# Performance work log

Measured on AMD Instinct MI355X. Metric: run time of the kernel, lower is better.

The kernel has to match this reference:

```python
import jax, jax.numpy as jnp
import numpy as np

N_NODES = 100000
N_EDGES = 1600000
D = 128
HID = 256  # min(2*D, 256)
D_OUT = 128
BN_EPS = 1e-5


def setup_inputs() -> dict:
    key = jax.random.key(0)
    ks = jax.random.split(key, 16)
    s = 0.05
    inp = {
        "x": jax.random.normal(ks[0], (N_NODES, D), dtype=jnp.float32),
        "edges": jax.random.randint(ks[1], (2, N_EDGES), 0, N_NODES, dtype=jnp.int32),
        # affine_before_rnn: Linear(D, D)
        "W_aff": jax.random.normal(ks[2], (D, D), dtype=jnp.float32) * s,
        "b_aff": jnp.zeros((D,), dtype=jnp.float32),
        # GRUCell(D, D)
        "W_ih": jax.random.normal(ks[3], (3 * D, D), dtype=jnp.float32) * s,
        "b_ih": jnp.zeros((3 * D,), dtype=jnp.float32),
        "W_hh": jax.random.normal(ks[4], (3 * D, D), dtype=jnp.float32) * s,
        "b_hh": jnp.zeros((3 * D,), dtype=jnp.float32),
        # merge_layer: Linear(2*D, D)
        "W_merge": jax.random.normal(ks[5], (D, 2 * D), dtype=jnp.float32) * s,
        "b_merge": jnp.zeros((D,), dtype=jnp.float32),
        # learnable self-connection weight
        "eps": jnp.asarray(1.0, dtype=jnp.float32),
        # backbone: Linear(D, HID) -> relu -> Linear(HID, D_OUT) -> relu -> BatchNorm1d
        "W1": jax.random.normal(ks[6], (HID, D), dtype=jnp.float32) * s,
        "b1": jnp.zeros((HID,), dtype=jnp.float32),
        "W2": jax.random.normal(ks[7], (D_OUT, HID), dtype=jnp.float32) * s,
        "b2": jnp.zeros((D_OUT,), dtype=jnp.float32),
        "gamma": jnp.ones((D_OUT,), dtype=jnp.float32),
        "beta": jnp.zeros((D_OUT,), dtype=jnp.float32),
    }
    return inp


def reference(x, edges, W_aff, b_aff, W_ih, b_ih, W_hh, b_hh,
              W_merge, b_merge, eps, W1, b1, W2, b2, gamma, beta):
    src, dst = edges[0], edges[1]
    n = x.shape[0]

    # ---- aggregation 1: 'sum' -> scatter-sum of neighbor features ----
    agg_sum = jax.ops.segment_sum(x[src], dst, num_segments=n)  # (N, D)

    # ---- aggregation 2: 'rnn-max' -> affine, scatter-max, GRUCell ----
    xi = x @ W_aff.T + b_aff
    agg_max = jax.ops.segment_max(xi[src], dst, num_segments=n)  # (N, D)
    agg_max = jnp.where(jnp.isfinite(agg_max), agg_max, 0.0)  # empty segments -> 0

    # GRUCell: input = aggregated neighbors, hidden = original node features
    gi = agg_max @ W_ih.T + b_ih  # (N, 3D)
    gh = x @ W_hh.T + b_hh        # (N, 3D)
    ir, iz, inn = jnp.split(gi, 3, axis=1)
    hr, hz, hn = jnp.split(gh, 3, axis=1)
    r = jax.nn.sigmoid(ir + hr)
    z = jax.nn.sigmoid(iz + hz)
    ncand = jnp.tanh(inn + r * hn)
    rnn_out = (1.0 - z) * ncand + z * x  # (N, D)

    # ---- merge ('cat') ----
    h = jnp.concatenate([agg_sum, rnn_out], axis=1) @ W_merge.T + b_merge  # (N, D)

    # ---- learnable self-connection ----
    h = h + eps * x

    # ---- backbone: dense -> relu -> dense -> relu -> batchnorm1d (train mode) ----
    h = jax.nn.relu(h @ W1.T + b1)
    h = jax.nn.relu(h @ W2.T + b2)
    mean = jnp.mean(h, axis=0)
    var = jnp.mean(jnp.square(h - mean), axis=0)  # biased batch variance
    out = gamma * (h - mean) * jax.lax.rsqrt(var + BN_EPS) + beta
    return out
```

## Files before the change

kernel.cpp:

```cpp
#include <hip/hip_runtime.h>
#include <hip/hip_bf16.h>
#include <math.h>

using bf16 = __hip_bfloat16;
typedef __attribute__((ext_vector_type(8))) short bf16x8;
typedef __attribute__((ext_vector_type(4))) float f32x4;

__device__ __forceinline__ float b2f(unsigned short u) {
  return __uint_as_float(((unsigned)u) << 16);
}
__device__ __forceinline__ unsigned short f2b(float f) {
  bf16 h = __float2bfloat16(f);
  return *reinterpret_cast<unsigned short*>(&h);
}
__device__ __forceinline__ ushort4 f2b4(float4 v) {
  return make_ushort4(f2b(v.x), f2b(v.y), f2b(v.z), f2b(v.w));
}

__global__ __launch_bounds__(256) void mgemm_k(
    const unsigned short* __restrict__ A, int lda, const float* __restrict__ W,
    const float* __restrict__ bias, unsigned short* __restrict__ Cb, int ldc,
    int N, int M, int K) {
  constexpr int LDA = 72;
  __shared__ unsigned short As[128 * LDA];
  __shared__ unsigned short Ws[128 * LDA];

  const int tid = threadIdx.x;
  const int lane = tid & 63;
  const int wave = tid >> 6;
  const int row0 = blockIdx.y * 128;
  const int m0 = blockIdx.x * 128;
  const int rowhalf = (wave & 1) * 64;
  const int colhalf = (wave >> 1) * 64;
  const int l15 = lane & 15;
  const int quad = lane >> 4;

  f32x4 acc[4][4] = {};

  for (int kc = 0; kc < K; kc += 64) {
#pragma unroll
    for (int i = 0; i < 4; i++) {
      int idx = tid + i * 256;
      int r = idx >> 3;
      int k8 = (idx & 7) * 8;
      int row = row0 + r;
      ushort4 u0 = make_ushort4(0, 0, 0, 0), u1 = u0;
      if (row < N) {
        const unsigned short* s = A + (size_t)row * lda + kc + k8;
        u0 = *(const ushort4*)s;
        u1 = *(const ushort4*)(s + 4);
      }
      *(ushort4*)&As[r * LDA + k8] = u0;
      *(ushort4*)&As[r * LDA + k8 + 4] = u1;
    }
#pragma unroll
    for (int i = 0; i < 8; i++) {
      int idx = tid + i * 256;
      int r = idx >> 4;
      int k4 = idx & 15;
      float4 v = *(const float4*)(W + (size_t)(m0 + r) * K + kc + k4 * 4);
      *(ushort4*)&Ws[r * LDA + k4 * 4] = f2b4(v);
    }
    __syncthreads();
#pragma unroll
    for (int ks = 0; ks < 2; ks++) {
      const int ko = ks * 32 + quad * 8;
      bf16x8 af[4], wf[4];
#pragma unroll
      for (int ri = 0; ri < 4; ri++)
        af[ri] = *(const bf16x8*)&As[(rowhalf + ri * 16 + l15) * LDA + ko];
#pragma unroll
      for (int ci = 0; ci < 4; ci++)
        wf[ci] = *(const bf16x8*)&Ws[(colhalf + ci * 16 + l15) * LDA + ko];
#pragma unroll
      for (int ri = 0; ri < 4; ri++)
#pragma unroll
        for (int ci = 0; ci < 4; ci++)
          acc[ri][ci] = __builtin_amdgcn_mfma_f32_16x16x32_bf16(
              af[ri], wf[ci], acc[ri][ci], 0, 0, 0);
    }
    __syncthreads();
  }
#pragma unroll
  for (int ci = 0; ci < 4; ci++) {
    const int col = m0 + colhalf + ci * 16 + l15;
    const float bv = bias[col];
#pragma unroll
    for (int ri = 0; ri < 4; ri++) {
      const int rbase = row0 + rowhalf + ri * 16 + quad * 4;
#pragma unroll
      for (int r = 0; r < 4; r++) {
        int row = rbase + r;
        if (row >= N) continue;
        Cb[(size_t)row * ldc + col] = f2b(acc[ri][ci][r] + bv);
      }
    }
  }
}

__global__ __launch_bounds__(256, 4) void grubb_k(
    const unsigned short* __restrict__ aggm,
    const unsigned short* __restrict__ xcat,
    const unsigned short* __restrict__ aggs,
    const unsigned short* __restrict__ Wbig,
    const float* __restrict__ bias_big,
    const unsigned short* __restrict__ Wmb, const float* __restrict__ bm,
    const unsigned short* __restrict__ W1b, const float* __restrict__ b1,
    const unsigned short* __restrict__ W2b, const float* __restrict__ b2,
    const float* __restrict__ epsp, float* __restrict__ out,
    float* __restrict__ pstats, int N) {
  constexpr int LDA = 264;
  constexpr int LDH = 136;
  __shared__ unsigned short As[32 * LDA];
  __shared__ unsigned short Acat[32 * LDA];
  __shared__ float sbn[128], qbn[128];
  unsigned short* Hd = As;
  unsigned short* Hp = Acat;

  const int tid = threadIdx.x;
  const int lane = tid & 63;
  const int wave = tid >> 6;
  const int l15 = lane & 15;
  const int quad = lane >> 4;
  const int row0 = blockIdx.x * 32;
  if (tid < 128) {
    sbn[tid] = 0.f;
    qbn[tid] = 0.f;
  }
  const float ep = epsp[0];

  {
    int r = tid >> 3;
    int k32 = (tid & 7) * 32;
    int row = row0 + r;
    uint4 u[4] = {};
    uint4 v[2] = {};
    if (row < N) {
      const unsigned short* s = (k32 < 128)
                                    ? aggm + (size_t)row * 128 + k32
                                    : xcat + (size_t)row * 256 + (k32 - 128);
#pragma unroll
      for (int i = 0; i < 4; i++) u[i] = *(const uint4*)(s + i * 8);
      const unsigned short* s2 = aggs + (size_t)row * 128 + (tid & 7) * 16;
      v[0] = *(const uint4*)s2;
      v[1] = *(const uint4*)(s2 + 8);
    }
#pragma unroll
    for (int i = 0; i < 4; i++) *(uint4*)&As[r * LDA + k32 + i * 8] = u[i];
    int k16 = (tid & 7) * 16;
    *(uint4*)&Acat[r * LDA + k16] = v[0];
    *(uint4*)&Acat[r * LDA + k16 + 8] = v[1];
  }
  __syncthreads();

  {
    const unsigned short* wptr =
        Wbig + (size_t)(wave * 128 + l15) * 256 + quad * 8;
    f32x4 acc[2][8] = {};
    bf16x8 wfA[4], wfB[4];
#pragma unroll
    for (int ci = 0; ci < 4; ci++)
      wfA[ci] = *(const bf16x8*)(wptr + ci * 16 * 256);
#pragma unroll
    for (int ks = 0; ks < 8; ks++) {
      const int ko = ks * 32 + quad * 8;
      bf16x8 af0 = *(const bf16x8*)&As[l15 * LDA + ko];
      bf16x8 af1 = *(const bf16x8*)&As[(16 + l15) * LDA + ko];
#pragma unroll
      for (int ci = 0; ci < 4; ci++)
        wfB[ci] = *(const bf16x8*)(wptr + (ci + 4) * 16 * 256 + ks * 32);
#pragma unroll
      for (int ci = 0; ci < 4; ci++) {
        acc[0][ci] = __builtin_amdgcn_mfma_f32_16x16x32_bf16(af0, wfA[ci],
                                                             acc[0][ci], 0, 0, 0);
        acc[1][ci] = __builtin_amdgcn_mfma_f32_16x16x32_bf16(af1, wfA[ci],
                                                             acc[1][ci], 0, 0, 0);
      }
      if (ks < 7) {
#pragma unroll
        for (int ci = 0; ci < 4; ci++)
          wfA[ci] = *(const bf16x8*)(wptr + ci * 16 * 256 + (ks + 1) * 32);
      }
#pragma unroll
      for (int ci = 0; ci < 4; ci++) {
        acc[0][4 + ci] = __builtin_amdgcn_mfma_f32_16x16x32_bf16(
            af0, wfB[ci], acc[0][4 + ci], 0, 0, 0);
        acc[1][4 + ci] = __builtin_amdgcn_mfma_f32_16x16x32_bf16(
            af1, wfB[ci], acc[1][4 + ci], 0, 0, 0);
      }
    }
#pragma unroll
    for (int fi = 0; fi < 2; fi++) {
      const int f = wave * 32 + fi * 16 + l15;
      const float br = bias_big[f];
      const float bz = bias_big[128 + f];
      const float bi = bias_big[256 + f];
      const float bh = bias_big[384 + f];
#pragma unroll
      for (int ri = 0; ri < 2; ri++) {
#pragma unroll
        for (int r = 0; r < 4; r++) {
          int rl = ri * 16 + quad * 4 + r;
          float rg = 1.f / (1.f + __expf(-(acc[ri][4 * fi + 0][r] + br)));
          float zg = 1.f / (1.f + __expf(-(acc[ri][4 * fi + 1][r] + bz)));
          float a =
              acc[ri][4 * fi + 2][r] + bi + rg * (acc[ri][4 * fi + 3][r] + bh);
          float t = 1.f - 2.f / (__expf(2.f * fabsf(a)) + 1.f);
          float nc = copysignf(t, a);
          float xv = b2f(As[rl * LDA + 128 + f]);
          Acat[rl * LDA + 128 + f] = f2b((1.f - zg) * nc + zg * xv);
        }
      }
    }
  }
  __syncthreads();

  f32x4 accm[2][2] = {};
  {
    const unsigned short* wptr =
        Wmb + (size_t)(wave * 32 + l15) * 256 + quad * 8;
    bf16x8 w0 = *(const bf16x8*)(wptr);
    bf16x8 w1 = *(const bf16x8*)(wptr + 16 * 256);
#pragma unroll
    for (int ks = 0; ks < 8; ks++) {
      const int ko = ks * 32 + quad * 8;
      bf16x8 af[2];
#pragma unroll
      for (int ri = 0; ri < 2; ri++)
        af[ri] = *(const bf16x8*)&Acat[(ri * 16 + l15) * LDA + ko];
      bf16x8 n0, n1;
      if (ks < 7) {
        n0 = *(const bf16x8*)(wptr + (ks + 1) * 32);
        n1 = *(const bf16x8*)(wptr + 16 * 256 + (ks + 1) * 32);
      }
#pragma unroll
      for (int ri = 0; ri < 2; ri++) {
        accm[ri][0] = __builtin_amdgcn_mfma_f32_16x16x32_bf16(af[ri], w0,
                                                              accm[ri][0], 0, 0, 0);
        accm[ri][1] = __builtin_amdgcn_mfma_f32_16x16x32_bf16(af[ri], w1,
                                                              accm[ri][1], 0, 0, 0);
      }
      if (ks < 7) {
        w0 = n0;
        w1 = n1;
      }
    }
  }
  __syncthreads();
  {
#pragma unroll
    for (int ci = 0; ci < 2; ci++) {
      int c = wave * 32 + ci * 16 + l15;
      float bv = bm[c];
#pragma unroll
      for (int ri = 0; ri < 2; ri++) {
#pragma unroll
        for (int r = 0; r < 4; r++) {
          int rl = ri * 16 + quad * 4 + r;
          float v = accm[ri][ci][r] + bv + ep * b2f(As[rl * LDA + 128 + c]);
          Hp[rl * LDH + c] = f2b(v);
        }
      }
    }
  }
  __syncthreads();

  f32x4 acc3[2][2] = {};
#pragma unroll
  for (int hh = 0; hh < 2; hh++) {
    f32x4 acc2[2][2] = {};
    {
      const unsigned short* wptr =
          W1b + (size_t)(hh * 128 + wave * 32 + l15) * 128 + quad * 8;
      bf16x8 w0 = *(const bf16x8*)(wptr);
      bf16x8 w1 = *(const bf16x8*)(wptr + 16 * 128);
#pragma unroll
      for (int ks = 0; ks < 4; ks++) {
        const int ko = ks * 32 + quad * 8;
        bf16x8 af[2];
#pragma unroll
        for (int ri = 0; ri < 2; ri++)
          af[ri] = *(const bf16x8*)&Hp[(ri * 16 + l15) * LDH + ko];
        bf16x8 n0, n1;
        if (ks < 3) {
          n0 = *(const bf16x8*)(wptr + (ks + 1) * 32);
          n1 = *(const bf16x8*)(wptr + 16 * 128 + (ks + 1) * 32);
        }
#pragma unroll
        for (int ri = 0; ri < 2; ri++) {
          acc2[ri][0] = __builtin_amdgcn_mfma_f32_16x16x32_bf16(
              af[ri], w0, acc2[ri][0], 0, 0, 0);
          acc2[ri][1] = __builtin_amdgcn_mfma_f32_16x16x32_bf16(
              af[ri], w1, acc2[ri][1], 0, 0, 0);
        }
        if (ks < 3) {
          w0 = n0;
          w1 = n1;
        }
      }
    }
    __syncthreads();
#pragma unroll
    for (int ci = 0; ci < 2; ci++) {
      int c = wave * 32 + ci * 16 + l15;
      float bv = b1[hh * 128 + c];
#pragma unroll
      for (int ri = 0; ri < 2; ri++) {
#pragma unroll
        for (int r = 0; r < 4; r++) {
          int rl = ri * 16 + quad * 4 + r;
          Hd[rl * LDH + c] = f2b(fmaxf(acc2[ri][ci][r] + bv, 0.f));
        }
      }
    }
    __syncthreads();
    {
      const unsigned short* wptr =
          W2b + (size_t)(wave * 32 + l15) * 256 + hh * 128 + quad * 8;
      bf16x8 w0 = *(const bf16x8*)(wptr);
      bf16x8 w1 = *(const bf16x8*)(wptr + 16 * 256);
#pragma unroll
      for (int ks = 0; ks < 4; ks++) {
        const int ko = ks * 32 + quad * 8;
        bf16x8 af[2];
#pragma unroll
        for (int ri = 0; ri < 2; ri++)
          af[ri] = *(const bf16x8*)&Hd[(ri * 16 + l15) * LDH + ko];
        bf16x8 n0, n1;
        if (ks < 3) {
          n0 = *(const bf16x8*)(wptr + (ks + 1) * 32);
          n1 = *(const bf16x8*)(wptr + 16 * 256 + (ks + 1) * 32);
        }
#pragma unroll
        for (int ri = 0; ri < 2; ri++) {
          acc3[ri][0] = __builtin_amdgcn_mfma_f32_16x16x32_bf16(
              af[ri], w0, acc3[ri][0], 0, 0, 0);
          acc3[ri][1] = __builtin_amdgcn_mfma_f32_16x16x32_bf16(
              af[ri], w1, acc3[ri][1], 0, 0, 0);
        }
        if (ks < 3) {
          w0 = n0;
          w1 = n1;
        }
      }
    }
  }
#pragma unroll
  for (int ci = 0; ci < 2; ci++) {
    int c = wave * 32 + ci * 16 + l15;
    float bv = b2[c];
    float s = 0.f, q = 0.f;
#pragma unroll
    for (int ri = 0; ri < 2; ri++) {
#pragma unroll
      for (int r = 0; r < 4; r++) {
        int rl = ri * 16 + quad * 4 + r;
        int row = row0 + rl;
        if (row >= N) continue;
        float v = fmaxf(acc3[ri][ci][r] + bv, 0.f);
        out[(size_t)row * 128 + c] = v;
        s += v;
        q += v * v;
      }
    }
    atomicAdd(&sbn[c], s);
    atomicAdd(&qbn[c], q);
  }
  __syncthreads();
  if (tid < 128) {
    float* p = pstats + (size_t)blockIdx.x * 256;
    p[tid] = sbn[tid];
    p[128 + tid] = qbn[tid];
  }
}

__global__ __launch_bounds__(256) void bnred_k(const float* __restrict__ pstats,
                                               float* __restrict__ stats,
                                               int nb) {
  int t = threadIdx.x;
  float s = 0.f;
  for (int b = blockIdx.x; b < nb; b += gridDim.x)
    s += pstats[(size_t)b * 256 + t];
  atomicAdd(&stats[t], s);
}

__global__ __launch_bounds__(256) void prep_k(
    const float* __restrict__ W_ih, const float* __restrict__ b_ih,
    const float* __restrict__ W_hh, const float* __restrict__ b_hh,
    const float* __restrict__ Wm, const float* __restrict__ W1,
    const float* __restrict__ W2, unsigned short* __restrict__ Wbig,
    unsigned short* __restrict__ Wmb, unsigned short* __restrict__ W1b,
    unsigned short* __restrict__ W2b, float* __restrict__ bias_big,
    float* __restrict__ stats, int* __restrict__ deg, int N) {
  int idx = blockIdx.x * 256 + threadIdx.x;
  if (idx < N) deg[idx] = 0;
  if (idx < 32768) {
    int mp = idx >> 6;
    int k4 = (idx & 63) * 4;
    int w = mp >> 7, ci = (mp >> 4) & 7, l15 = mp & 15;
    int g = ci & 3, fi = ci >> 2;
    int f = w * 32 + fi * 16 + l15;
    const float* src = nullptr;
    int koff = 0;
    if (g <= 1) {
      int m = g * 128 + f;
      if (k4 < 128) { src = W_ih + (size_t)m * 128; koff = k4; }
      else          { src = W_hh + (size_t)m * 128; koff = k4 - 128; }
    } else if (g == 2) {
      if (k4 < 128) { src = W_ih + (size_t)(256 + f) * 128; koff = k4; }
    } else {
      if (k4 >= 128) { src = W_hh + (size_t)(256 + f) * 128; koff = k4 - 128; }
    }
    ushort4 o = make_ushort4(0, 0, 0, 0);
    if (src) o = f2b4(*(const float4*)(src + koff));
    *(ushort4*)&Wbig[(size_t)mp * 256 + k4] = o;
  }
  if (idx < 8192) {
    int m = idx >> 6;
    int k4 = (idx & 63) * 4;
    *(ushort4*)&Wmb[(size_t)m * 256 + k4] =
        f2b4(*(const float4*)(Wm + (size_t)m * 256 + k4));
    *(ushort4*)&W2b[(size_t)m * 256 + k4] =
        f2b4(*(const float4*)(W2 + (size_t)m * 256 + k4));
    int m2 = idx >> 5;
    int k42 = (idx & 31) * 4;
    *(ushort4*)&W1b[(size_t)m2 * 128 + k42] =
        f2b4(*(const float4*)(W1 + (size_t)m2 * 128 + k42));
  }
  if (blockIdx.x == 0) {
    int t = threadIdx.x;
    stats[t] = 0.f;
#pragma unroll
    for (int h = 0; h < 2; h++) {
      int mm = t + h * 256;
      float b;
      if (mm < 256) b = b_ih[mm] + b_hh[mm];
      else if (mm < 384) b = b_ih[mm];
      else b = b_hh[mm - 128];
      bias_big[mm] = b;
    }
  }
}

__global__ __launch_bounds__(256) void cvthist_k(
    const int* __restrict__ edges, int* __restrict__ deg, int E,
    const float* __restrict__ x, unsigned short* __restrict__ xcat,
    int ngroups, int eblk) {
  if ((int)blockIdx.x < eblk) {
    int e = blockIdx.x * 256 + threadIdx.x;
    if (e < E) atomicAdd(&deg[edges[(size_t)E + e]], 1);
  } else {
    int g = (blockIdx.x - eblk) * 256 + threadIdx.x;
    if (g >= ngroups) return;
    int n = g >> 5;
    int j = (g & 31) * 4;
    float4 v = *(const float4*)&x[(size_t)n * 128 + j];
    *(ushort4*)&xcat[(size_t)n * 256 + j] = f2b4(v);
  }
}

__global__ __launch_bounds__(256) void scan1_k(const int* __restrict__ deg,
                                               int* __restrict__ off,
                                               int* __restrict__ bsums, int N) {
  __shared__ int s[256];
  int t = threadIdx.x;
  int i = blockIdx.x * 256 + t;
  int v = (i < N) ? deg[i] : 0;
  s[t] = v;
  __syncthreads();
#pragma unroll
  for (int d = 1; d < 256; d <<= 1) {
    int u = (t >= d) ? s[t - d] : 0;
    __syncthreads();
    s[t] += u;
    __syncthreads();
  }
  if (i < N) off[i] = s[t] - v;
  if (t == 255) bsums[blockIdx.x] = s[255];
}

__global__ __launch_bounds__(512) void scan2_k(int* __restrict__ bsums,
                                               int nb) {
  __shared__ int s[512];
  int t = threadIdx.x;
  int v = (t < nb) ? bsums[t] : 0;
  s[t] = v;
  __syncthreads();
#pragma unroll
  for (int d = 1; d < 512; d <<= 1) {
    int u = (t >= d) ? s[t - d] : 0;
    __syncthreads();
    s[t] += u;
    __syncthreads();
  }
  if (t < nb) bsums[t] = s[t] - v;
}

__global__ __launch_bounds__(256) void scan3_k(int* __restrict__ off,
                                               const int* __restrict__ bsums,
                                               int* __restrict__ binoff,
                                               int* __restrict__ bincur,
                                               int N, int E, int NB) {
  int i = blockIdx.x * 256 + threadIdx.x;
  if (i < N) {
    int o = off[i] + bsums[blockIdx.x];
    off[i] = o;
    if ((i & 511) == 0) {
      binoff[i >> 9] = o;
      bincur[i >> 9] = o;
    }
  }
  if (i == 0) {
    off[N] = E;
    binoff[NB] = E;
  }
}

__global__ __launch_bounds__(256) void edgepart_k(const int* __restrict__ edges,
                                                  int* __restrict__ bincur,
                                                  int* __restrict__ part,
                                                  int E, int NB) {
  __shared__ int cnt[256];
  const int tid = threadIdx.x;
  if (tid < NB) cnt[tid] = 0;
  __syncthreads();
  int sv[16], dv[16];
  const int e0 = blockIdx.x * 4096;
#pragma unroll
  for (int i = 0; i < 16; i++) {
    int e = e0 + i * 256 + tid;
    int s = 0, d = -1;
    if (e < E) {
      s = edges[e];
      d = edges[(size_t)E + e];
    }
    sv[i] = s;
    dv[i] = d;
    if (d >= 0) atomicAdd(&cnt[d >> 9], 1);
  }
  __syncthreads();
  if (tid < NB) {
    int c = cnt[tid];
    int base = c ? atomicAdd(&bincur[tid], c) : 0;
    cnt[tid] = base;
  }
  __syncthreads();
#pragma unroll
  for (int i = 0; i < 16; i++) {
    int d = dv[i];
    if (d < 0) continue;
    int p = atomicAdd(&cnt[d >> 9], 1);
    part[p] = (sv[i] << 9) | (d & 511);
  }
}

__global__ __launch_bounds__(1024) void fill2_k(const int* __restrict__ off,
                                                const int* __restrict__ binoff,
                                                const int* __restrict__ part,
                                                int* __restrict__ bucket,
                                                int N) {
  __shared__ int scur[512];
  const int b = blockIdx.x;
  const int n0 = b << 9;
  const int tid = threadIdx.x;
  if (tid < 512) {
    int node = n0 + tid;
    scur[tid] = (node < N) ? off[node] : 0;
  }
  __syncthreads();
  const int j0 = binoff[b];
  const int j1 = binoff[b + 1];
  for (int j = j0 + tid; j < j1; j += 1024) {
    int p = part[j];
    int pos = atomicAdd(&scur[p & 511], 1);
    bucket[pos] = p >> 9;
  }
}

__global__ __launch_bounds__(256) void gather_k(
    const int* __restrict__ off, const int* __restrict__ bucket,
    const unsigned short* __restrict__ xcat, unsigned short* __restrict__ aggm,
    unsigned short* __restrict__ aggs, int N) {
  int node = blockIdx.x * 4 + (threadIdx.x >> 6);
  if (node >= N) return;
  const int lane = threadIdx.x & 63;
  const int half = lane >> 5;
  const int f = (lane & 31) * 4;
  const int j0 = off[node], jend = off[node + 1];
  float s0 = 0.f, s1 = 0.f, s2 = 0.f, s3 = 0.f;
  float m0 = -INFINITY, m1 = -INFINITY, m2 = -INFINITY, m3 = -INFINITY;
  int jj = j0 + half;
  int p0 = (jj < jend) ? bucket[jj] : 0;
  int p1 = (jj + 2 < jend) ? bucket[jj + 2] : 0;
  for (; jj < jend; jj += 2) {
    int src = p0;
    p0 = p1;
    p1 = (jj + 4 < jend) ? bucket[jj + 4] : 0;
    ushort4 a = *(const ushort4*)(xcat + (size_t)src * 256 + f);
    ushort4 b = *(const ushort4*)(xcat + (size_t)src * 256 + 128 + f);
    s0 += b2f(a.x);
    s1 += b2f(a.y);
    s2 += b2f(a.z);
    s3 += b2f(a.w);
    m0 = fmaxf(m0, b2f(b.x));
    m1 = fmaxf(m1, b2f(b.y));
    m2 = fmaxf(m2, b2f(b.z));
    m3 = fmaxf(m3, b2f(b.w));
  }
  s0 += __shfl_xor(s0, 32);
  s1 += __shfl_xor(s1, 32);
  s2 += __shfl_xor(s2, 32);
  s3 += __shfl_xor(s3, 32);
  m0 = fmaxf(m0, __shfl_xor(m0, 32));
  m1 = fmaxf(m1, __shfl_xor(m1, 32));
  m2 = fmaxf(m2, __shfl_xor(m2, 32));
  m3 = fmaxf(m3, __shfl_xor(m3, 32));
  if (half == 0) {
    bool nz = jend > j0;
    ushort4 mv = nz ? make_ushort4(f2b(m0), f2b(m1), f2b(m2), f2b(m3))
                    : make_ushort4(0, 0, 0, 0);
    *(ushort4*)&aggm[(size_t)node * 128 + f] = mv;
    *(ushort4*)&aggs[(size_t)node * 128 + f] =
        make_ushort4(f2b(s0), f2b(s1), f2b(s2), f2b(s3));
  }
}

__global__ __launch_bounds__(256) void bn_apply_k(
    float* __restrict__ out, const float* __restrict__ stats,
    const float* __restrict__ gamma, const float* __restrict__ beta,
    float invn, int nd4) {
  int g = blockIdx.x * 256 + threadIdx.x;
  if (g >= nd4) return;
  int d = (g & 31) * 4;
  float4 v = ((float4*)out)[g];
  float o[4] = {v.x, v.y, v.z, v.w};
#pragma unroll
  for (int i = 0; i < 4; i++) {
    float mean = stats[d + i] * invn;
    float var = fmaxf(stats[128 + d + i] * invn - mean * mean, 0.f);
    float sc = gamma[d + i] * rsqrtf(var + 1e-5f);
    o[i] = (o[i] - mean) * sc + beta[d + i];
  }
  ((float4*)out)[g] = make_float4(o[0], o[1], o[2], o[3]);
}

extern "C" void kernel_launch(void* const* d_in, const int* in_sizes, int n_in,
                              void* d_out, int out_size, void* d_ws,
                              size_t ws_size, hipStream_t stream) {
  (void)n_in;
  (void)out_size;
  (void)ws_size;
  const float* x = (const float*)d_in[0];
  const int* edges = (const int*)d_in[1];
  const float* W_aff = (const float*)d_in[2];
  const float* b_aff = (const float*)d_in[3];
  const float* W_ih = (const float*)d_in[4];
  const float* b_ih = (const float*)d_in[5];
  const float* W_hh = (const float*)d_in[6];
  const float* b_hh = (const float*)d_in[7];
  const float* W_merge = (const float*)d_in[8];
  const float* b_merge = (const float*)d_in[9];
  const float* epsp = (const float*)d_in[10];
  const float* W1 = (const float*)d_in[11];
  const float* b1 = (const float*)d_in[12];
  const float* W2 = (const float*)d_in[13];
  const float* b2 = (const float*)d_in[14];
  const float* gamma = (const float*)d_in[15];
  const float* beta = (const float*)d_in[16];

  const int N = in_sizes[0] / 128;
  const int E = in_sizes[1] / 2;
  const size_t nd = (size_t)N * 128;
  const int NB = (N + 511) >> 9;
  const int gblk = (N + 31) / 32;

  char* base = (char*)d_ws;
  unsigned short* xcat = (unsigned short*)base;
  unsigned short* aggs = (unsigned short*)(base + (size_t)N * 512);
  unsigned short* aggm = (unsigned short*)(base + (size_t)N * 1024);
  unsigned short* Wbig = (unsigned short*)(base + (size_t)N * 1280);
  unsigned short* Wmb = Wbig + 512 * 256;
  unsigned short* W1b = Wmb + 128 * 256;
  unsigned short* W2b = W1b + 256 * 128;
  float* bias_big = (float*)(W2b + 128 * 256);
  float* stats = bias_big + 512;
  int* deg = (int*)(stats + 512);
  int* off = deg + N;
  int* binoff = off + N + 1;
  int* bincur = binoff + NB + 1;
  int* bucket = bincur + NB;
  int* bsums = bucket + E;
  float* pstats = (float*)(bsums + ((N + 255) / 256));
  float* out = (float*)d_out;
  int* part = (int*)d_out;

  const int ny = (N + 127) / 128;
  const int nblk = (N + 255) / 256;
  const int eblk = (E + 255) / 256;
  const int cvtblk = (int)((nd / 4 + 255) / 256);
  const int pgrid = nblk > 128 ? nblk : 128;
  dim3 blk(256);

  prep_k<<<pgrid, blk, 0, stream>>>(W_ih, b_ih, W_hh, b_hh, W_merge, W1, W2,
                                    Wbig, Wmb, W1b, W2b, bias_big, stats, deg,
                                    N);
  cvthist_k<<<eblk + cvtblk, blk, 0, stream>>>(edges, deg, E, x, xcat,
                                               (int)(nd / 4), eblk);
  scan1_k<<<nblk, blk, 0, stream>>>(deg, off, bsums, N);
  scan2_k<<<1, 512, 0, stream>>>(bsums, nblk);
  scan3_k<<<nblk, blk, 0, stream>>>(off, bsums, binoff, bincur, N, E, NB);
  edgepart_k<<<(E + 4095) / 4096, blk, 0, stream>>>(edges, bincur, part, E, NB);
  fill2_k<<<NB, dim3(1024), 0, stream>>>(off, binoff, part, bucket, N);

  mgemm_k<<<dim3(1, ny), blk, 0, stream>>>(xcat, 256, W_aff, b_aff, xcat + 128,
                                           256, N, 128, 128);
  gather_k<<<(N + 3) / 4, blk, 0, stream>>>(off, bucket, xcat, aggm, aggs, N);
  grubb_k<<<gblk, blk, 0, stream>>>(aggm, xcat, aggs, Wbig, bias_big,
                                    Wmb, b_merge, W1b, b1, W2b, b2,
                                    epsp, out, pstats, N);
  bnred_k<<<64, blk, 0, stream>>>(pstats, stats, gblk);
  bn_apply_k<<<(int)((nd / 4 + 255) / 256), blk, 0, stream>>>(
      out, stats, gamma, beta, 1.f / (float)N, (int)(nd / 4));
}
```

Measured before the change: 631.9 us.

## Double row tile of fused GRU/MLP kernel to 64 rows and skip zero gate blocks

```diff
diff --git a/kernel.cpp b/kernel.cpp
--- a/kernel.cpp
+++ b/kernel.cpp
@@ -98,7 +98,7 @@
   }
 }
 
-__global__ __launch_bounds__(256, 4) void grubb_k(
+__global__ __launch_bounds__(256, 2) void grubb_k(
     const unsigned short* __restrict__ aggm,
     const unsigned short* __restrict__ xcat,
     const unsigned short* __restrict__ aggs,
@@ -111,8 +111,8 @@
     float* __restrict__ pstats, int N) {
   constexpr int LDA = 264;
   constexpr int LDH = 136;
-  __shared__ unsigned short As[32 * LDA];
-  __shared__ unsigned short Acat[32 * LDA];
+  __shared__ unsigned short As[64 * LDA];
+  __shared__ unsigned short Acat[64 * LDA];
   __shared__ float sbn[128], qbn[128];
   unsigned short* Hd = As;
   unsigned short* Hp = Acat;
@@ -122,7 +122,7 @@
   const int wave = tid >> 6;
   const int l15 = lane & 15;
   const int quad = lane >> 4;
-  const int row0 = blockIdx.x * 32;
+  const int row0 = blockIdx.x * 64;
   if (tid < 128) {
     sbn[tid] = 0.f;
     qbn[tid] = 0.f;
@@ -130,63 +130,50 @@
   const float ep = epsp[0];
 
   {
-    int r = tid >> 3;
-    int k32 = (tid & 7) * 32;
+    int r = tid >> 2;
+    int q = tid & 3;
     int row = row0 + r;
-    uint4 u[4] = {};
-    uint4 v[2] = {};
+    int k64 = q * 64;
+    uint4 u[8] = {};
+    uint4 v[4] = {};
     if (row < N) {
-      const unsigned short* s = (k32 < 128)
-                                    ? aggm + (size_t)row * 128 + k32
-                                    : xcat + (size_t)row * 256 + (k32 - 128);
-#pragma unroll
-      for (int i = 0; i < 4; i++) u[i] = *(const uint4*)(s + i * 8);
-      const unsigned short* s2 = aggs + (size_t)row * 128 + (tid & 7) * 16;
-      v[0] = *(const uint4*)s2;
-      v[1] = *(const uint4*)(s2 + 8);
-    }
-#pragma unroll
-    for (int i = 0; i < 4; i++) *(uint4*)&As[r * LDA + k32 + i * 8] = u[i];
-    int k16 = (tid & 7) * 16;
-    *(uint4*)&Acat[r * LDA + k16] = v[0];
-    *(uint4*)&Acat[r * LDA + k16 + 8] = v[1];
+      const unsigned short* s = (k64 < 128)
+                                    ? aggm + (size_t)row * 128 + k64
+                                    : xcat + (size_t)row * 256 + (k64 - 128);
+#pragma unroll
+      for (int i = 0; i < 8; i++) u[i] = *(const uint4*)(s + i * 8);
+      const unsigned short* s2 = aggs + (size_t)row * 128 + q * 32;
+#pragma unroll
+      for (int i = 0; i < 4; i++) v[i] = *(const uint4*)(s2 + i * 8);
+    }
+#pragma unroll
+    for (int i = 0; i < 8; i++) *(uint4*)&As[r * LDA + k64 + i * 8] = u[i];
+#pragma unroll
+    for (int i = 0; i < 4; i++) *(uint4*)&Acat[r * LDA + q * 32 + i * 8] = v[i];
   }
   __syncthreads();
 
   {
     const unsigned short* wptr =
         Wbig + (size_t)(wave * 128 + l15) * 256 + quad * 8;
-    f32x4 acc[2][8] = {};
-    bf16x8 wfA[4], wfB[4];
-#pragma unroll
-    for (int ci = 0; ci < 4; ci++)
-      wfA[ci] = *(const bf16x8*)(wptr + ci * 16 * 256);
+    f32x4 acc[4][8] = {};
 #pragma unroll
     for (int ks = 0; ks < 8; ks++) {
       const int ko = ks * 32 + quad * 8;
-      bf16x8 af0 = *(const bf16x8*)&As[l15 * LDA + ko];
-      bf16x8 af1 = *(const bf16x8*)&As[(16 + l15) * LDA + ko];
-#pragma unroll
-      for (int ci = 0; ci < 4; ci++)
-        wfB[ci] = *(const bf16x8*)(wptr + (ci + 4) * 16 * 256 + ks * 32);
-#pragma unroll
-      for (int ci = 0; ci < 4; ci++) {
-        acc[0][ci] = __builtin_amdgcn_mfma_f32_16x16x32_bf16(af0, wfA[ci],
-                                                             acc[0][ci], 0, 0, 0);
-        acc[1][ci] = __builtin_amdgcn_mfma_f32_16x16x32_bf16(af1, wfA[ci],
-                                                             acc[1][ci], 0, 0, 0);
-      }
-      if (ks < 7) {
-#pragma unroll
-        for (int ci = 0; ci < 4; ci++)
-          wfA[ci] = *(const bf16x8*)(wptr + ci * 16 * 256 + (ks + 1) * 32);
-      }
-#pragma unroll
-      for (int ci = 0; ci < 4; ci++) {
-        acc[0][4 + ci] = __builtin_amdgcn_mfma_f32_16x16x32_bf16(
-            af0, wfB[ci], acc[0][4 + ci], 0, 0, 0);
-        acc[1][4 + ci] = __builtin_amdgcn_mfma_f32_16x16x32_bf16(
-            af1, wfB[ci], acc[1][4 + ci], 0, 0, 0);
+      bf16x8 af[4];
+#pragma unroll
+      for (int ri = 0; ri < 4; ri++)
+        af[ri] = *(const bf16x8*)&As[(ri * 16 + l15) * LDA + ko];
+#pragma unroll
+      for (int ci = 0; ci < 8; ci++) {
+        const int g = ci & 3;
+        if (g == 2 && ks >= 4) continue;
+        if (g == 3 && ks < 4) continue;
+        bf16x8 wf = *(const bf16x8*)(wptr + (size_t)ci * 16 * 256 + ks * 32);
+#pragma unroll
+        for (int ri = 0; ri < 4; ri++)
+          acc[ri][ci] = __builtin_amdgcn_mfma_f32_16x16x32_bf16(
+              af[ri], wf, acc[ri][ci], 0, 0, 0);
       }
     }
 #pragma unroll
@@ -197,7 +184,7 @@
       const float bi = bias_big[256 + f];
       const float bh = bias_big[384 + f];
 #pragma unroll
-      for (int ri = 0; ri < 2; ri++) {
+      for (int ri = 0; ri < 4; ri++) {
 #pragma unroll
         for (int r = 0; r < 4; r++) {
           int rl = ri * 16 + quad * 4 + r;
@@ -215,35 +202,26 @@
   }
   __syncthreads();
 
-  f32x4 accm[2][2] = {};
+  f32x4 accm[4][2] = {};
   {
     const unsigned short* wptr =
         Wmb + (size_t)(wave * 32 + l15) * 256 + quad * 8;
-    bf16x8 w0 = *(const bf16x8*)(wptr);
-    bf16x8 w1 = *(const bf16x8*)(wptr + 16 * 256);
 #pragma unroll
     for (int ks = 0; ks < 8; ks++) {
       const int ko = ks * 32 + quad * 8;
-      bf16x8 af[2];
-#pragma unroll
-      for (int ri = 0; ri < 2; ri++)
+      bf16x8 af[4];
+#pragma unroll
+      for (int ri = 0; ri < 4; ri++)
         af[ri] = *(const bf16x8*)&Acat[(ri * 16 + l15) * LDA + ko];
-      bf16x8 n0, n1;
-      if (ks < 7) {
-        n0 = *(const bf16x8*)(wptr + (ks + 1) * 32);
-        n1 = *(const bf16x8*)(wptr + 16 * 256 + (ks + 1) * 32);
-      }
-#pragma unroll
-      for (int ri = 0; ri < 2; ri++) {
+      bf16x8 w0 = *(const bf16x8*)(wptr + ks * 32);
+      bf16x8 w1 = *(const bf16x8*)(wptr + 16 * 256 + ks * 32);
+#pragma unroll
+      for (int ri = 0; ri < 4; ri++) {
         accm[ri][0] = __builtin_amdgcn_mfma_f32_16x16x32_bf16(af[ri], w0,
                                                               accm[ri][0], 0, 0, 0);
         accm[ri][1] = __builtin_amdgcn_mfma_f32_16x16x32_bf16(af[ri], w1,
                                                               accm[ri][1], 0, 0, 0);
       }
-      if (ks < 7) {
-        w0 = n0;
-        w1 = n1;
-      }
     }
   }
   __syncthreads();
@@ -253,7 +231,7 @@
       int c = wave * 32 + ci * 16 + l15;
       float bv = bm[c];
 #pragma unroll
-      for (int ri = 0; ri < 2; ri++) {
+      for (int ri = 0; ri < 4; ri++) {
 #pragma unroll
         for (int r = 0; r < 4; r++) {
           int rl = ri * 16 + quad * 4 + r;
@@ -265,38 +243,29 @@
   }
   __syncthreads();
 
-  f32x4 acc3[2][2] = {};
+  f32x4 acc3[4][2] = {};
 #pragma unroll
   for (int hh = 0; hh < 2; hh++) {
-    f32x4 acc2[2][2] = {};
+    f32x4 acc2[4][2] = {};
     {
       const unsigned short* wptr =
           W1b + (size_t)(hh * 128 + wave * 32 + l15) * 128 + quad * 8;
-      bf16x8 w0 = *(const bf16x8*)(wptr);
-      bf16x8 w1 = *(const bf16x8*)(wptr + 16 * 128);
 #pragma unroll
       for (int ks = 0; ks < 4; ks++) {
         const int ko = ks * 32 + quad * 8;
-        bf16x8 af[2];
-#pragma unroll
-        for (int ri = 0; ri < 2; ri++)
+        bf16x8 af[4];
+#pragma unroll
+        for (int ri = 0; ri < 4; ri++)
           af[ri] = *(const bf16x8*)&Hp[(ri * 16 + l15) * LDH + ko];
-        bf16x8 n0, n1;
-        if (ks < 3) {
-          n0 = *(const bf16x8*)(wptr + (ks + 1) * 32);
-          n1 = *(const bf16x8*)(wptr + 16 * 128 + (ks + 1) * 32);
-        }
-#pragma unroll
-        for (int ri = 0; ri < 2; ri++) {
+        bf16x8 w0 = *(const bf16x8*)(wptr + ks * 32);
+        bf16x8 w1 = *(const bf16x8*)(wptr + 16 * 128 + ks * 32);
+#pragma unroll
+        for (int ri = 0; ri < 4; ri++) {
           acc2[ri][0] = __builtin_amdgcn_mfma_f32_16x16x32_bf16(
               af[ri], w0, acc2[ri][0], 0, 0, 0);
           acc2[ri][1] = __builtin_amdgcn_mfma_f32_16x16x32_bf16(
               af[ri], w1, acc2[ri][1], 0, 0, 0);
         }
-        if (ks < 3) {
-          w0 = n0;
-          w1 = n1;
-        }
       }
     }
     __syncthreads();
@@ -305,7 +274,7 @@
       int c = wave * 32 + ci * 16 + l15;
       float bv = b1[hh * 128 + c];
 #pragma unroll
-      for (int ri = 0; ri < 2; ri++) {
+      for (int ri = 0; ri < 4; ri++) {
 #pragma unroll
         for (int r = 0; r < 4; r++) {
           int rl = ri * 16 + quad * 4 + r;
@@ -317,31 +286,22 @@
     {
       const unsigned short* wptr =
           W2b + (size_t)(wave * 32 + l15) * 256 + hh * 128 + quad * 8;
-      bf16x8 w0 = *(const bf16x8*)(wptr);
-      bf16x8 w1 = *(const bf16x8*)(wptr + 16 * 256);
 #pragma unroll
       for (int ks = 0; ks < 4; ks++) {
         const int ko = ks * 32 + quad * 8;
-        bf16x8 af[2];
-#pragma unroll
-        for (int ri = 0; ri < 2; ri++)
+        bf16x8 af[4];
+#pragma unroll
+        for (int ri = 0; ri < 4; ri++)
           af[ri] = *(const bf16x8*)&Hd[(ri * 16 + l15) * LDH + ko];
-        bf16x8 n0, n1;
-        if (ks < 3) {
-          n0 = *(const bf16x8*)(wptr + (ks + 1) * 32);
-          n1 = *(const bf16x8*)(wptr + 16 * 256 + (ks + 1) * 32);
-        }
-#pragma unroll
-        for (int ri = 0; ri < 2; ri++) {
+        bf16x8 w0 = *(const bf16x8*)(wptr + ks * 32);
+        bf16x8 w1 = *(const bf16x8*)(wptr + 16 * 256 + ks * 32);
+#pragma unroll
+        for (int ri = 0; ri < 4; ri++) {
           acc3[ri][0] = __builtin_amdgcn_mfma_f32_16x16x32_bf16(
               af[ri], w0, acc3[ri][0], 0, 0, 0);
           acc3[ri][1] = __builtin_amdgcn_mfma_f32_16x16x32_bf16(
               af[ri], w1, acc3[ri][1], 0, 0, 0);
         }
-        if (ks < 3) {
-          w0 = n0;
-          w1 = n1;
-        }
       }
     }
   }
@@ -351,7 +311,7 @@
     float bv = b2[c];
     float s = 0.f, q = 0.f;
 #pragma unroll
-    for (int ri = 0; ri < 2; ri++) {
+    for (int ri = 0; ri < 4; ri++) {
 #pragma unroll
       for (int r = 0; r < 4; r++) {
         int rl = ri * 16 + quad * 4 + r;
@@ -672,7 +632,7 @@
   const int E = in_sizes[1] / 2;
   const size_t nd = (size_t)N * 128;
   const int NB = (N + 511) >> 9;
-  const int gblk = (N + 31) / 32;
+  const int gblk = (N + 63) / 64;
 
   char* base = (char*)d_ws;
   unsigned short* xcat = (unsigned short*)base;
```

Result: faster. 563.3 us (-10.9%).
